# Optimization experiments

Measured on AMD Instinct MI355X. Metric: run time of the kernel, lower is better.

## Reference

```python
import jax, jax.numpy as jnp
import numpy as np

N_ITEMS = 100000
N_USERS = 16384
HIST = 50
TEXT_DIM = 256
GCN_DIM = 128
HIDDEN_DIM = 512
TOWER_DIM = 128


def _l2norm(x, eps=1e-12):
    # F.normalize(dim=1): x / max(||x||, eps)
    n = jnp.sqrt(jnp.sum(x * x, axis=1, keepdims=True))
    return x / jnp.maximum(n, eps)


def setup_inputs() -> dict:
    key = jax.random.key(0)
    ks = jax.random.split(key, 10)
    s1i = 1.0 / np.sqrt(TEXT_DIM + GCN_DIM)
    s2i = 1.0 / np.sqrt(HIDDEN_DIM)
    s1u = 1.0 / np.sqrt(GCN_DIM + TOWER_DIM)
    return {
        "item_text_emb": jax.random.normal(ks[0], (N_ITEMS, TEXT_DIM), jnp.float32),
        "gcn_item_emb": jax.random.normal(ks[1], (N_ITEMS, GCN_DIM), jnp.float32),
        "gcn_user_emb": jax.random.normal(ks[2], (N_USERS, GCN_DIM), jnp.float32),
        "hist_idx": jax.random.randint(ks[3], (N_USERS, HIST), 0, N_ITEMS),
        "W1i": jax.random.normal(ks[4], (TEXT_DIM + GCN_DIM, HIDDEN_DIM), jnp.float32) * s1i,
        "b1i": jnp.zeros((HIDDEN_DIM,), jnp.float32),
        "W2i": jax.random.normal(ks[5], (HIDDEN_DIM, TOWER_DIM), jnp.float32) * s2i,
        "b2i": jnp.zeros((TOWER_DIM,), jnp.float32),
        "W1u": jax.random.normal(ks[6], (GCN_DIM + TOWER_DIM, HIDDEN_DIM), jnp.float32) * s1u,
        "b1u": jnp.zeros((HIDDEN_DIM,), jnp.float32),
        "W2u": jax.random.normal(ks[7], (HIDDEN_DIM, TOWER_DIM), jnp.float32) * s2i,
        "b2u": jnp.zeros((TOWER_DIM,), jnp.float32),
    }


def reference(item_text_emb, gcn_item_emb, gcn_user_emb, hist_idx,
              W1i, b1i, W2i, b2i, W1u, b1u, W2u, b2u):
    # encode_items: MLP over concat(text, gcn) features, then L2 normalize
    item_feat = jnp.concatenate([item_text_emb, gcn_item_emb], axis=1)  # [N_items, text+gcn]
    h = jax.nn.relu(item_feat @ W1i + b1i)
    item_emb = _l2norm(h @ W2i + b2i)  # [N_items, TOWER_DIM]
    # encode_users: per-user gather of history item embeddings + mean pooling
    hist = jnp.mean(item_emb[hist_idx], axis=1)  # [N_users, TOWER_DIM]
    fused = jnp.concatenate([gcn_user_emb, hist], axis=1)
    hu = jax.nn.relu(fused @ W1u + b1u)
    user_emb = _l2norm(hu @ W2u + b2u)  # [N_users, TOWER_DIM]
    return user_emb
```

## Files before the change

### kernel.cpp

```cpp
#include <hip/hip_runtime.h>
#include <hip/hip_bf16.h>

#define HIST 50
#define N_ITEMS 100000
#define N_USERS 16384

typedef __bf16 bf8 __attribute__((ext_vector_type(8)));
typedef float  f4  __attribute__((ext_vector_type(4)));

__device__ __forceinline__ unsigned short f2bf(float x) {
    unsigned u = __builtin_bit_cast(unsigned, x);
    u += 0x7fffu + ((u >> 16) & 1u);
    return (unsigned short)(u >> 16);
}
__device__ __forceinline__ float bf2f(unsigned b) {
    unsigned u = b << 16;
    return __builtin_bit_cast(float, u);
}

__global__ void pack_weights(const float* __restrict__ W1i, const float* __restrict__ W2i,
                             const float* __restrict__ W1u, const float* __restrict__ W2u,
                             unsigned short* __restrict__ dstbase)
{
    int i = blockIdx.x * 256 + threadIdx.x;
    const float* W; unsigned short* dst; int N, KS, loc;
    if (i < 24576)      { W = W1i; dst = dstbase;          N = 512; KS = 12; loc = i; }
    else if (i < 32768) { W = W2i; dst = dstbase + 196608; N = 128; KS = 16; loc = i - 24576; }
    else if (i < 49152) { W = W1u; dst = dstbase + 262144; N = 512; KS = 8;  loc = i - 32768; }
    else                { W = W2u; dst = dstbase + 393216; N = 128; KS = 16; loc = i - 49152; }
    int l = loc & 63, fi = loc >> 6;
    int ks = fi % KS, nt = fi / KS;
    int q = l >> 4, c = l & 15;
    const float* src = W + (size_t)(ks * 32 + q * 8) * N + nt * 16 + c;
    unsigned o[4];
    #pragma unroll
    for (int k = 0; k < 4; ++k) {
        unsigned lo = f2bf(src[(2 * k) * N]);
        unsigned hi = f2bf(src[(2 * k + 1) * N]);
        o[k] = lo | (hi << 16);
    }
    uint4 v; v.x = o[0]; v.y = o[1]; v.z = o[2]; v.w = o[3];
    ((uint4*)dst)[(size_t)(nt * KS + ks) * 64 + l] = v;
}

template<int KS1, int ASTR, bool OUT_BF16>
__device__ __forceinline__ void tower_core(
    unsigned short* U, const float* b1s, const float* b2s, float* sumsq,
    const bf8* __restrict__ w1f, const bf8* __restrict__ w2f,
    void* __restrict__ outp, int row0, int nval, int tid)
{
    const int HSTR = 520;
    const int l = tid & 63, w = tid >> 6;
    const int q = l >> 4, c = l & 15;

    f4 acc1[4][8];
    #pragma unroll
    for (int i = 0; i < 4; ++i)
        #pragma unroll
        for (int j = 0; j < 8; ++j) acc1[i][j] = (f4)0.0f;

    const unsigned short* ap = U + c * ASTR + q * 8;
    #pragma unroll
    for (int ks = 0; ks < KS1; ++ks) {
        bf8 a[4], b[8];
        #pragma unroll
        for (int rt = 0; rt < 4; ++rt)
            a[rt] = *(const bf8*)(ap + rt * 16 * ASTR + ks * 32);
        #pragma unroll
        for (int nt = 0; nt < 8; ++nt)
            b[nt] = w1f[(size_t)((w * 8 + nt) * KS1 + ks) * 64 + l];
        #pragma unroll
        for (int rt = 0; rt < 4; ++rt)
            #pragma unroll
            for (int nt = 0; nt < 8; ++nt)
                acc1[rt][nt] = __builtin_amdgcn_mfma_f32_16x16x32_bf16(a[rt], b[nt], acc1[rt][nt], 0, 0, 0);
    }
    __syncthreads();

    #pragma unroll
    for (int nt = 0; nt < 8; ++nt) {
        int col = w * 128 + nt * 16 + c;
        float bias = b1s[col];
        #pragma unroll
        for (int rt = 0; rt < 4; ++rt)
            #pragma unroll
            for (int reg = 0; reg < 4; ++reg) {
                float h = fmaxf(acc1[rt][nt][reg] + bias, 0.0f);
                U[(rt * 16 + q * 4 + reg) * HSTR + col] = f2bf(h);
            }
    }
    __syncthreads();

    f4 acc2[4][2];
    #pragma unroll
    for (int i = 0; i < 4; ++i)
        #pragma unroll
        for (int j = 0; j < 2; ++j) acc2[i][j] = (f4)0.0f;

    const unsigned short* hp = U + c * HSTR + q * 8;
    #pragma unroll
    for (int ks = 0; ks < 16; ++ks) {
        bf8 a[4], b[2];
        #pragma unroll
        for (int rt = 0; rt < 4; ++rt)
            a[rt] = *(const bf8*)(hp + rt * 16 * HSTR + ks * 32);
        #pragma unroll
        for (int j = 0; j < 2; ++j)
            b[j] = w2f[(size_t)((w * 2 + j) * 16 + ks) * 64 + l];
        #pragma unroll
        for (int rt = 0; rt < 4; ++rt)
            #pragma unroll
            for (int j = 0; j < 2; ++j)
                acc2[rt][j] = __builtin_amdgcn_mfma_f32_16x16x32_bf16(a[rt], b[j], acc2[rt][j], 0, 0, 0);
    }

    float v[4][2][4];
    #pragma unroll
    for (int rt = 0; rt < 4; ++rt)
        #pragma unroll
        for (int j = 0; j < 2; ++j) {
            float bias = b2s[w * 32 + j * 16 + c];
            #pragma unroll
            for (int reg = 0; reg < 4; ++reg)
                v[rt][j][reg] = acc2[rt][j][reg] + bias;
        }
    #pragma unroll
    for (int rt = 0; rt < 4; ++rt)
        #pragma unroll
        for (int reg = 0; reg < 4; ++reg) {
            float s = v[rt][0][reg] * v[rt][0][reg] + v[rt][1][reg] * v[rt][1][reg];
            s += __shfl_xor(s, 1); s += __shfl_xor(s, 2);
            s += __shfl_xor(s, 4); s += __shfl_xor(s, 8);
            if (c == 0) atomicAdd(&sumsq[rt * 16 + q * 4 + reg], s);
        }
    __syncthreads();
    #pragma unroll
    for (int rt = 0; rt < 4; ++rt)
        #pragma unroll
        for (int reg = 0; reg < 4; ++reg) {
            int row = rt * 16 + q * 4 + reg;
            if (row < nval) {
                float inv = 1.0f / fmaxf(sqrtf(sumsq[row]), 1e-12f);
                #pragma unroll
                for (int j = 0; j < 2; ++j) {
                    int col = w * 32 + j * 16 + c;
                    float o = v[rt][j][reg] * inv;
                    if (OUT_BF16)
                        ((unsigned short*)outp)[(size_t)(row0 + row) * 128 + col] = f2bf(o);
                    else
                        ((float*)outp)[(size_t)(row0 + row) * 128 + col] = o;
                }
            }
        }
}

#define ASI 392
#define ASU 264

__global__ __launch_bounds__(256, 2) void item_kernel(
    const float* __restrict__ text, const float* __restrict__ gcn,
    const bf8* __restrict__ w1f, const float* __restrict__ b1,
    const bf8* __restrict__ w2f, const float* __restrict__ b2,
    unsigned short* __restrict__ item_bf)
{
    __shared__ __align__(16) unsigned short U[64 * 520];
    __shared__ float b1s[512], b2s[128], sumsq[64];
    const int tid = threadIdx.x;
    const int row0 = blockIdx.x * 64;
    const int nval = min(64, N_ITEMS - row0);
    const float4* t4 = (const float4*)text;
    const float4* g4 = (const float4*)gcn;
    #pragma unroll
    for (int j = 0; j < 16; ++j) {
        int idx = tid + j * 256; int r = idx >> 6, c4 = idx & 63;
        float4 x = (r < nval) ? t4[(size_t)(row0 + r) * 64 + c4] : make_float4(0.f,0.f,0.f,0.f);
        ushort4 s; s.x = f2bf(x.x); s.y = f2bf(x.y); s.z = f2bf(x.z); s.w = f2bf(x.w);
        *(ushort4*)(U + r * ASI + c4 * 4) = s;
    }
    #pragma unroll
    for (int j = 0; j < 8; ++j) {
        int idx = tid + j * 256; int r = idx >> 5, c4 = idx & 31;
        float4 x = (r < nval) ? g4[(size_t)(row0 + r) * 32 + c4] : make_float4(0.f,0.f,0.f,0.f);
        ushort4 s; s.x = f2bf(x.x); s.y = f2bf(x.y); s.z = f2bf(x.z); s.w = f2bf(x.w);
        *(ushort4*)(U + r * ASI + 256 + c4 * 4) = s;
    }
    b1s[tid] = b1[tid]; b1s[tid + 256] = b1[tid + 256];
    if (tid < 128) b2s[tid] = b2[tid];
    if (tid < 64)  sumsq[tid] = 0.0f;
    __syncthreads();
    tower_core<12, ASI, true>(U, b1s, b2s, sumsq, w1f, w2f, item_bf, row0, nval, tid);
}

__global__ __launch_bounds__(256, 2) void user_kernel(
    const float* __restrict__ gcnu, const int* __restrict__ hist,
    const unsigned short* __restrict__ item_bf,
    const bf8* __restrict__ w1f, const float* __restrict__ b1,
    const bf8* __restrict__ w2f, const float* __restrict__ b2,
    float* __restrict__ outp)
{
    __shared__ __align__(16) unsigned short U[64 * 520];
    __shared__ float b1s[512], b2s[128], sumsq[64];
    const int tid = threadIdx.x;
    const int u0 = blockIdx.x * 64;
    const float4* g4 = (const float4*)gcnu;
    #pragma unroll
    for (int j = 0; j < 8; ++j) {
        int idx = tid + j * 256; int r = idx >> 5, c4 = idx & 31;
        float4 x = g4[(size_t)(u0 + r) * 32 + c4];
        ushort4 s; s.x = f2bf(x.x); s.y = f2bf(x.y); s.z = f2bf(x.z); s.w = f2bf(x.w);
        *(ushort4*)(U + r * ASU + c4 * 4) = s;
    }
    b1s[tid] = b1[tid]; b1s[tid + 256] = b1[tid + 256];
    if (tid < 128) b2s[tid] = b2[tid];
    if (tid < 64)  sumsq[tid] = 0.0f;
    {
        const int u = tid >> 2, g = tid & 3;
        float f[32];
        #pragma unroll
        for (int k = 0; k < 32; ++k) f[k] = 0.0f;
        const int* hrow = hist + (size_t)(u0 + u) * HIST;
        #pragma unroll 5
        for (int t = 0; t < HIST; ++t) {
            int id = hrow[t];
            const uint4* p = (const uint4*)(item_bf + (size_t)id * 128 + g * 32);
            #pragma unroll
            for (int h = 0; h < 4; ++h) {
                uint4 x = p[h];
                unsigned vs[4] = {x.x, x.y, x.z, x.w};
                #pragma unroll
                for (int k = 0; k < 4; ++k) {
                    f[h * 8 + 2 * k]     += bf2f(vs[k] & 0xffffu);
                    f[h * 8 + 2 * k + 1] += bf2f(vs[k] >> 16);
                }
            }
        }
        unsigned o[16];
        #pragma unroll
        for (int k = 0; k < 16; ++k)
            o[k] = (unsigned)f2bf(f[2 * k] * 0.02f) | ((unsigned)f2bf(f[2 * k + 1] * 0.02f) << 16);
        unsigned short* dstp = U + u * ASU + 128 + g * 32;
        #pragma unroll
        for (int h = 0; h < 4; ++h) {
            uint4 s; s.x = o[h*4]; s.y = o[h*4+1]; s.z = o[h*4+2]; s.w = o[h*4+3];
            *(uint4*)(dstp + h * 8) = s;
        }
    }
    __syncthreads();
    tower_core<8, ASU, false>(U, b1s, b2s, sumsq, w1f, w2f, outp, u0, 64, tid);
}

extern "C" void kernel_launch(void* const* d_in, const int* in_sizes, int n_in,
                              void* d_out, int out_size, void* d_ws, size_t ws_size,
                              hipStream_t stream) {
    const float* text = (const float*)d_in[0];
    const float* gcni = (const float*)d_in[1];
    const float* gcnu = (const float*)d_in[2];
    const int*   hist = (const int*)d_in[3];
    const float* W1i  = (const float*)d_in[4];
    const float* b1i  = (const float*)d_in[5];
    const float* W2i  = (const float*)d_in[6];
    const float* b2i  = (const float*)d_in[7];
    const float* W1u  = (const float*)d_in[8];
    const float* b1u  = (const float*)d_in[9];
    const float* W2u  = (const float*)d_in[10];
    const float* b2u  = (const float*)d_in[11];
    float* out = (float*)d_out;

    unsigned short* itemb = (unsigned short*)d_ws;
    unsigned short* pw = itemb + 12800000;

    pack_weights<<<224, 256, 0, stream>>>(W1i, W2i, W1u, W2u, pw);
    item_kernel<<<(N_ITEMS + 63) / 64, 256, 0, stream>>>(
        text, gcni, (const bf8*)pw, b1i, (const bf8*)(pw + 196608), b2i, itemb);
    user_kernel<<<N_USERS / 64, 256, 0, stream>>>(
        gcnu, hist, itemb, (const bf8*)(pw + 262144), b1u, (const bf8*)(pw + 393216), b2u, out);
}
```

Measured before the change: 343.3 us.

## Double block size to 512 threads, split MFMA tiles across eight waves

Both tower kernels now run 8 waves per 64-row block instead of 4. In GEMM1 each wave covers 64 hidden columns instead of 128, and in GEMM2 the 64x128 output is split into 2 row groups by 4 column groups. The history gather uses 8 threads per user instead of 4. This cuts accumulator registers per thread to raise occupancy and latency hiding, at the cost of more shared-memory A-tile reads per block. Launch bounds become (512,4), which LDS size (~66KB per block) likely cannot satisfy.

```diff
diff --git a/kernel.cpp b/kernel.cpp
--- a/kernel.cpp
+++ b/kernel.cpp
@@ -53,33 +53,33 @@
     const int l = tid & 63, w = tid >> 6;
     const int q = l >> 4, c = l & 15;
 
-    f4 acc1[4][8];
+    f4 acc1[4][4];
     #pragma unroll
     for (int i = 0; i < 4; ++i)
         #pragma unroll
-        for (int j = 0; j < 8; ++j) acc1[i][j] = (f4)0.0f;
+        for (int j = 0; j < 4; ++j) acc1[i][j] = (f4)0.0f;
 
     const unsigned short* ap = U + c * ASTR + q * 8;
     #pragma unroll
     for (int ks = 0; ks < KS1; ++ks) {
-        bf8 a[4], b[8];
+        bf8 a[4], b[4];
         #pragma unroll
         for (int rt = 0; rt < 4; ++rt)
             a[rt] = *(const bf8*)(ap + rt * 16 * ASTR + ks * 32);
         #pragma unroll
-        for (int nt = 0; nt < 8; ++nt)
-            b[nt] = w1f[(size_t)((w * 8 + nt) * KS1 + ks) * 64 + l];
+        for (int nt = 0; nt < 4; ++nt)
+            b[nt] = w1f[(size_t)((w * 4 + nt) * KS1 + ks) * 64 + l];
         #pragma unroll
         for (int rt = 0; rt < 4; ++rt)
             #pragma unroll
-            for (int nt = 0; nt < 8; ++nt)
+            for (int nt = 0; nt < 4; ++nt)
                 acc1[rt][nt] = __builtin_amdgcn_mfma_f32_16x16x32_bf16(a[rt], b[nt], acc1[rt][nt], 0, 0, 0);
     }
     __syncthreads();
 
     #pragma unroll
-    for (int nt = 0; nt < 8; ++nt) {
-        int col = w * 128 + nt * 16 + c;
+    for (int nt = 0; nt < 4; ++nt) {
+        int col = w * 64 + nt * 16 + c;
         float bias = b1s[col];
         #pragma unroll
         for (int rt = 0; rt < 4; ++rt)
@@ -91,60 +91,61 @@
     }
     __syncthreads();
 
-    f4 acc2[4][2];
-    #pragma unroll
-    for (int i = 0; i < 4; ++i)
+    const int rg = w >> 2, jj = w & 3;
+    f4 acc2[2][2];
+    #pragma unroll
+    for (int i = 0; i < 2; ++i)
         #pragma unroll
         for (int j = 0; j < 2; ++j) acc2[i][j] = (f4)0.0f;
 
-    const unsigned short* hp = U + c * HSTR + q * 8;
+    const unsigned short* hp = U + (size_t)(rg * 32 + c) * HSTR + q * 8;
     #pragma unroll
     for (int ks = 0; ks < 16; ++ks) {
-        bf8 a[4], b[2];
-        #pragma unroll
-        for (int rt = 0; rt < 4; ++rt)
-            a[rt] = *(const bf8*)(hp + rt * 16 * HSTR + ks * 32);
+        bf8 a[2], b[2];
+        #pragma unroll
+        for (int i = 0; i < 2; ++i)
+            a[i] = *(const bf8*)(hp + i * 16 * HSTR + ks * 32);
         #pragma unroll
         for (int j = 0; j < 2; ++j)
-            b[j] = w2f[(size_t)((w * 2 + j) * 16 + ks) * 64 + l];
-        #pragma unroll
-        for (int rt = 0; rt < 4; ++rt)
+            b[j] = w2f[(size_t)((jj * 2 + j) * 16 + ks) * 64 + l];
+        #pragma unroll
+        for (int i = 0; i < 2; ++i)
             #pragma unroll
             for (int j = 0; j < 2; ++j)
-                acc2[rt][j] = __builtin_amdgcn_mfma_f32_16x16x32_bf16(a[rt], b[j], acc2[rt][j], 0, 0, 0);
-    }
-
-    float v[4][2][4];
-    #pragma unroll
-    for (int rt = 0; rt < 4; ++rt)
+                acc2[i][j] = __builtin_amdgcn_mfma_f32_16x16x32_bf16(a[i], b[j], acc2[i][j], 0, 0, 0);
+    }
+
+    float v[2][2][4];
+    #pragma unroll
+    for (int i = 0; i < 2; ++i)
         #pragma unroll
         for (int j = 0; j < 2; ++j) {
-            float bias = b2s[w * 32 + j * 16 + c];
+            float bias = b2s[jj * 32 + j * 16 + c];
             #pragma unroll
             for (int reg = 0; reg < 4; ++reg)
-                v[rt][j][reg] = acc2[rt][j][reg] + bias;
-        }
-    #pragma unroll
-    for (int rt = 0; rt < 4; ++rt)
+                v[i][j][reg] = acc2[i][j][reg] + bias;
+        }
+    #pragma unroll
+    for (int i = 0; i < 2; ++i)
         #pragma unroll
         for (int reg = 0; reg < 4; ++reg) {
-            float s = v[rt][0][reg] * v[rt][0][reg] + v[rt][1][reg] * v[rt][1][reg];
+            float s = v[i][0][reg] * v[i][0][reg] + v[i][1][reg] * v[i][1][reg];
             s += __shfl_xor(s, 1); s += __shfl_xor(s, 2);
             s += __shfl_xor(s, 4); s += __shfl_xor(s, 8);
-            if (c == 0) atomicAdd(&sumsq[rt * 16 + q * 4 + reg], s);
-        }
-    __syncthreads();
-    #pragma unroll
-    for (int rt = 0; rt < 4; ++rt)
+            if (c == 0) atomicAdd(&sumsq[rg * 32 + i * 16 + q * 4 + reg], s);
+        }
+    __syncthreads();
+    #pragma unroll
+    for (int i = 0; i < 2; ++i)
         #pragma unroll
         for (int reg = 0; reg < 4; ++reg) {
-            int row = rt * 16 + q * 4 + reg;
+            int row = rg * 32 + i * 16 + q * 4 + reg;
             if (row < nval) {
                 float inv = 1.0f / fmaxf(sqrtf(sumsq[row]), 1e-12f);
                 #pragma unroll
                 for (int j = 0; j < 2; ++j) {
-                    int col = w * 32 + j * 16 + c;
-                    float o = v[rt][j][reg] * inv;
+                    int col = jj * 32 + j * 16 + c;
+                    float o = v[i][j][reg] * inv;
                     if (OUT_BF16)
                         ((unsigned short*)outp)[(size_t)(row0 + row) * 128 + col] = f2bf(o);
                     else
@@ -157,7 +158,7 @@
 #define ASI 392
 #define ASU 264
 
-__global__ __launch_bounds__(256, 2) void item_kernel(
+__global__ __launch_bounds__(512, 4) void item_kernel(
     const float* __restrict__ text, const float* __restrict__ gcn,
     const bf8* __restrict__ w1f, const float* __restrict__ b1,
     const bf8* __restrict__ w2f, const float* __restrict__ b2,
@@ -171,27 +172,27 @@
     const float4* t4 = (const float4*)text;
     const float4* g4 = (const float4*)gcn;
     #pragma unroll
-    for (int j = 0; j < 16; ++j) {
-        int idx = tid + j * 256; int r = idx >> 6, c4 = idx & 63;
+    for (int j = 0; j < 8; ++j) {
+        int idx = tid + j * 512; int r = idx >> 6, c4 = idx & 63;
         float4 x = (r < nval) ? t4[(size_t)(row0 + r) * 64 + c4] : make_float4(0.f,0.f,0.f,0.f);
         ushort4 s; s.x = f2bf(x.x); s.y = f2bf(x.y); s.z = f2bf(x.z); s.w = f2bf(x.w);
         *(ushort4*)(U + r * ASI + c4 * 4) = s;
     }
     #pragma unroll
-    for (int j = 0; j < 8; ++j) {
-        int idx = tid + j * 256; int r = idx >> 5, c4 = idx & 31;
+    for (int j = 0; j < 4; ++j) {
+        int idx = tid + j * 512; int r = idx >> 5, c4 = idx & 31;
         float4 x = (r < nval) ? g4[(size_t)(row0 + r) * 32 + c4] : make_float4(0.f,0.f,0.f,0.f);
         ushort4 s; s.x = f2bf(x.x); s.y = f2bf(x.y); s.z = f2bf(x.z); s.w = f2bf(x.w);
         *(ushort4*)(U + r * ASI + 256 + c4 * 4) = s;
     }
-    b1s[tid] = b1[tid]; b1s[tid + 256] = b1[tid + 256];
+    b1s[tid] = b1[tid];
     if (tid < 128) b2s[tid] = b2[tid];
     if (tid < 64)  sumsq[tid] = 0.0f;
     __syncthreads();
     tower_core<12, ASI, true>(U, b1s, b2s, sumsq, w1f, w2f, item_bf, row0, nval, tid);
 }
 
-__global__ __launch_bounds__(256, 2) void user_kernel(
+__global__ __launch_bounds__(512, 4) void user_kernel(
     const float* __restrict__ gcnu, const int* __restrict__ hist,
     const unsigned short* __restrict__ item_bf,
     const bf8* __restrict__ w1f, const float* __restrict__ b1,
@@ -204,27 +205,27 @@
     const int u0 = blockIdx.x * 64;
     const float4* g4 = (const float4*)gcnu;
     #pragma unroll
-    for (int j = 0; j < 8; ++j) {
-        int idx = tid + j * 256; int r = idx >> 5, c4 = idx & 31;
+    for (int j = 0; j < 4; ++j) {
+        int idx = tid + j * 512; int r = idx >> 5, c4 = idx & 31;
         float4 x = g4[(size_t)(u0 + r) * 32 + c4];
         ushort4 s; s.x = f2bf(x.x); s.y = f2bf(x.y); s.z = f2bf(x.z); s.w = f2bf(x.w);
         *(ushort4*)(U + r * ASU + c4 * 4) = s;
     }
-    b1s[tid] = b1[tid]; b1s[tid + 256] = b1[tid + 256];
+    b1s[tid] = b1[tid];
     if (tid < 128) b2s[tid] = b2[tid];
     if (tid < 64)  sumsq[tid] = 0.0f;
     {
-        const int u = tid >> 2, g = tid & 3;
-        float f[32];
-        #pragma unroll
-        for (int k = 0; k < 32; ++k) f[k] = 0.0f;
+        const int u = tid >> 3, g = tid & 7;
+        float f[16];
+        #pragma unroll
+        for (int k = 0; k < 16; ++k) f[k] = 0.0f;
         const int* hrow = hist + (size_t)(u0 + u) * HIST;
         #pragma unroll 5
         for (int t = 0; t < HIST; ++t) {
             int id = hrow[t];
-            const uint4* p = (const uint4*)(item_bf + (size_t)id * 128 + g * 32);
-            #pragma unroll
-            for (int h = 0; h < 4; ++h) {
+            const uint4* p = (const uint4*)(item_bf + (size_t)id * 128 + g * 16);
+            #pragma unroll
+            for (int h = 0; h < 2; ++h) {
                 uint4 x = p[h];
                 unsigned vs[4] = {x.x, x.y, x.z, x.w};
                 #pragma unroll
@@ -234,13 +235,13 @@
                 }
             }
         }
-        unsigned o[16];
-        #pragma unroll
-        for (int k = 0; k < 16; ++k)
+        unsigned o[8];
+        #pragma unroll
+        for (int k = 0; k < 8; ++k)
             o[k] = (unsigned)f2bf(f[2 * k] * 0.02f) | ((unsigned)f2bf(f[2 * k + 1] * 0.02f) << 16);
-        unsigned short* dstp = U + u * ASU + 128 + g * 32;
-        #pragma unroll
-        for (int h = 0; h < 4; ++h) {
+        unsigned short* dstp = U + u * ASU + 128 + g * 16;
+        #pragma unroll
+        for (int h = 0; h < 2; ++h) {
             uint4 s; s.x = o[h*4]; s.y = o[h*4+1]; s.z = o[h*4+2]; s.w = o[h*4+3];
             *(uint4*)(dstp + h * 8) = s;
         }
@@ -270,8 +271,8 @@
     unsigned short* pw = itemb + 12800000;
 
     pack_weights<<<224, 256, 0, stream>>>(W1i, W2i, W1u, W2u, pw);
-    item_kernel<<<(N_ITEMS + 63) / 64, 256, 0, stream>>>(
+    item_kernel<<<(N_ITEMS + 63) / 64, 512, 0, stream>>>(
         text, gcni, (const bf8*)pw, b1i, (const bf8*)(pw + 196608), b2i, itemb);
-    user_kernel<<<N_USERS / 64, 256, 0, stream>>>(
+    user_kernel<<<N_USERS / 64, 512, 0, stream>>>(
         gcnu, hist, itemb, (const bf8*)(pw + 262144), b1u, (const bf8*)(pw + 393216), b2u, out);
 }
```

Measured after the change: 320.9 us. 1.07x faster.
